# Performance work log

Measured on AMD Instinct MI355X. Metric: run time of the kernel, lower is better.

The kernel has to match this reference:

```python
import jax, jax.numpy as jnp
import numpy as np

HIDDEN = 2048
NUM_HEADS = 32
GROUP_SIZE = 4
HEAD_DIM = HIDDEN // NUM_HEADS            # 64
GROUP_NUM = NUM_HEADS // GROUP_SIZE       # 8 KV heads
B, S = 2, 2048


def setup_inputs() -> dict:
    key = jax.random.key(0)
    ks = jax.random.split(key, 7)
    sc = 1.0 / np.sqrt(HIDDEN)
    x = jax.random.normal(ks[0], (B, S, HIDDEN), dtype=jnp.float32)
    attention_mask = jnp.ones((B, S), dtype=jnp.int32)
    Wq = jax.random.normal(ks[1], (HIDDEN, HIDDEN), dtype=jnp.float32) * sc
    bq = jax.random.normal(ks[2], (HIDDEN,), dtype=jnp.float32) * 0.02
    Wk = jax.random.normal(ks[3], (HIDDEN, GROUP_NUM * HEAD_DIM), dtype=jnp.float32) * sc
    bk = jax.random.normal(ks[4], (GROUP_NUM * HEAD_DIM,), dtype=jnp.float32) * 0.02
    Wv = jax.random.normal(ks[5], (HIDDEN, GROUP_NUM * HEAD_DIM), dtype=jnp.float32) * sc
    bv = jax.random.normal(ks[6], (GROUP_NUM * HEAD_DIM,), dtype=jnp.float32) * 0.02
    return {"x": x, "attention_mask": attention_mask,
            "Wq": Wq, "bq": bq, "Wk": Wk, "bk": bk, "Wv": Wv, "bv": bv}


def reference(x, attention_mask, Wq, bq, Wk, bk, Wv, bv):
    b, s, _ = x.shape
    # projections
    q = (x @ Wq + bq).reshape(b, s, NUM_HEADS, HEAD_DIM).transpose(0, 2, 1, 3)   # (B,H,S,hd)
    k = (x @ Wk + bk).reshape(b, s, GROUP_NUM, HEAD_DIM).transpose(0, 2, 1, 3)   # (B,G,S,hd)
    v = (x @ Wv + bv).reshape(b, s, GROUP_NUM, HEAD_DIM).transpose(0, 2, 1, 3)
    # expand KV groups to full head count (head h uses group h // group_size)
    k = jnp.repeat(k, GROUP_SIZE, axis=1)                                        # (B,H,S,hd)
    v = jnp.repeat(v, GROUP_SIZE, axis=1)
    # NOTE: original torch code uses floor-division `//` for scaling and no softmax
    score = jnp.floor(jnp.einsum('bhqd,bhkd->bhqk', q, k) / np.sqrt(HEAD_DIM).astype(np.float32))
    score = jnp.where(attention_mask[:, None, None, :] == 0, -jnp.inf, score)
    out = jnp.einsum('bhqk,bhkd->bhqd', score, v)                                # (B,H,S,hd)
    return out.transpose(0, 2, 1, 3).reshape(b, s, HIDDEN)
```

## Files before the change

kernel.cpp:

```cpp
#include <hip/hip_runtime.h>
#include <math.h>

#define HIDDEN 2048
#define NHEADS 32
#define HDIM 64
#define GNUM 8
#define KVDIM 512
#define BB 2
#define SS 2048
#define MROWS (BB * SS)
#define NQKV 3072

typedef _Float16 half8 __attribute__((ext_vector_type(8)));
typedef _Float16 half4 __attribute__((ext_vector_type(4)));
typedef _Float16 half2 __attribute__((ext_vector_type(2)));
typedef __fp16 fp16x2 __attribute__((ext_vector_type(2)));
typedef float floatx4 __attribute__((ext_vector_type(4)));

#define MFMA16(a, b, c) __builtin_amdgcn_mfma_f32_16x16x32_f16((a), (b), (c), 0, 0, 0)

__device__ __forceinline__ void split_f32(float x, _Float16& hi, _Float16& lo) {
    hi = (_Float16)x;
    lo = (_Float16)((x - (float)hi) * 2048.0f);
}

__device__ __forceinline__ void load_lds16(const void* g, void* l) {
    __builtin_amdgcn_global_load_lds(
        (const __attribute__((address_space(1))) void*)g,
        (__attribute__((address_space(3))) void*)l, 16, 0, 0);
}

__device__ __forceinline__ void permswap32(unsigned& a, unsigned& b) {
    asm volatile("v_permlane32_swap_b32 %0, %1" : "+v"(a), "+v"(b));
}
__device__ __forceinline__ void permswap16(unsigned& a, unsigned& b) {
    asm volatile("v_permlane16_swap_b32 %0, %1" : "+v"(a), "+v"(b));
}

__device__ __forceinline__ unsigned pk_f16(float a, float b) {
    union { fp16x2 h; unsigned u; } c;
    c.h = __builtin_amdgcn_cvt_pkrtz(a, b);
    return c.u;
}

__global__ __launch_bounds__(256)
void split_x(const float* __restrict__ x, _Float16* __restrict__ xh,
             _Float16* __restrict__ xl, int n4) {
    for (int idx = blockIdx.x * 256 + threadIdx.x; idx < n4; idx += gridDim.x * 256) {
        floatx4 v = reinterpret_cast<const floatx4*>(x)[idx];
        half4 h, l;
        #pragma unroll
        for (int e = 0; e < 4; ++e) { _Float16 hi, lo; split_f32(v[e], hi, lo); h[e] = hi; l[e] = lo; }
        reinterpret_cast<half4*>(xh)[idx] = h;
        reinterpret_cast<half4*>(xl)[idx] = l;
    }
}

__global__ __launch_bounds__(256)
void split_wt(const float* __restrict__ W, int N, int n0,
              _Float16* __restrict__ Wth, _Float16* __restrict__ Wtl) {
    __shared__ float tile[64][68];
    const int tid = threadIdx.x;
    const int kb = blockIdx.x, nb = blockIdx.y;
    #pragma unroll
    for (int i = 0; i < 4; ++i) {
        int idx = tid + i * 256;
        int r = idx >> 4, c4 = idx & 15;
        floatx4 v = *reinterpret_cast<const floatx4*>(&W[(size_t)(kb * 64 + r) * N + nb * 64 + c4 * 4]);
        *reinterpret_cast<floatx4*>(&tile[r][c4 * 4]) = v;
    }
    __syncthreads();
    #pragma unroll
    for (int i = 0; i < 4; ++i) {
        int idx = tid + i * 256;
        int r2 = idx >> 4, c2 = (idx & 15) * 4;
        half4 h, l;
        #pragma unroll
        for (int e = 0; e < 4; ++e) {
            _Float16 hi, lo;
            split_f32(tile[c2 + e][r2], hi, lo);
            h[e] = hi; l[e] = lo;
        }
        size_t o = (size_t)(n0 + nb * 64 + r2) * HIDDEN + kb * 64 + c2;
        *reinterpret_cast<half4*>(&Wth[o]) = h;
        *reinterpret_cast<half4*>(&Wtl[o]) = l;
    }
}

__global__ __launch_bounds__(256)
void biascat_k(const float* __restrict__ bq, const float* __restrict__ bk,
               const float* __restrict__ bv, float* __restrict__ bias) {
    int i = blockIdx.x * 256 + threadIdx.x;
    if (i < 2048) bias[i] = bq[i];
    else if (i < 2560) bias[i] = bk[i - 2048];
    else if (i < NQKV) bias[i] = bv[i - 2560];
}

__global__ __launch_bounds__(256, 2)
void gemm_qkv(const _Float16* __restrict__ xh, const _Float16* __restrict__ xl,
              const _Float16* __restrict__ Wth, const _Float16* __restrict__ Wtl,
              const float* __restrict__ bias,
              _Float16* __restrict__ qh, _Float16* __restrict__ ql,
              _Float16* __restrict__ khs, _Float16* __restrict__ kls,
              _Float16* __restrict__ vhs) {
    __shared__ __align__(16) _Float16 Ah[128 * 64];
    __shared__ __align__(16) _Float16 Al[128 * 64];
    __shared__ __align__(16) _Float16 Bh[128 * 64];
    __shared__ __align__(16) _Float16 Bl[128 * 64];

    const int tid  = threadIdx.x;
    const int lane = tid & 63;
    const int w    = tid >> 6;
    const int wm   = w >> 1, wn = w & 1;
    const int bm   = blockIdx.x, bn = blockIdx.y;
    const int ml   = lane & 15;
    const int kg8  = (lane >> 4) * 8;
    const bool lo3 = (bn < 20);

    const _Float16* gsrc;
    _Float16* ldst;
    if      (w == 0) { gsrc = xh  + (size_t)(bm * 128) * HIDDEN; ldst = Ah; }
    else if (w == 1) { gsrc = xl  + (size_t)(bm * 128) * HIDDEN; ldst = Al; }
    else if (w == 2) { gsrc = Wth + (size_t)(bn * 128) * HIDDEN; ldst = Bh; }
    else             { gsrc = Wtl + (size_t)(bn * 128) * HIDDEN; ldst = Bl; }
    const bool do_stage = lo3 || (w == 0) || (w == 2);

    floatx4 acc0[4][4] = {};
    floatx4 accL[4][4] = {};

    for (int k0 = 0; k0 < HIDDEN; k0 += 64) {
        if (do_stage) {
            #pragma unroll
            for (int i = 0; i < 16; ++i) {
                int L   = i * 1024 + lane * 16;
                int row = L >> 7;
                int off = (L & 127) ^ ((row & 7) << 4);
                const void* gp = (const char*)(gsrc + (size_t)row * HIDDEN + k0) + off;
                void* lp = (char*)ldst + i * 1024;
                load_lds16(gp, lp);
            }
        }
        __syncthreads();

        #pragma unroll
        for (int kc = 0; kc < 2; ++kc) {
            half8 a_h[4], b_h[4];
            #pragma unroll
            for (int r = 0; r < 4; ++r) {
                int row = wm * 64 + r * 16 + ml;
                int byt = row * 128 + (((kc * 64 + kg8 * 2)) ^ ((row & 7) << 4));
                a_h[r] = *reinterpret_cast<const half8*>((const char*)Ah + byt);
            }
            #pragma unroll
            for (int c = 0; c < 4; ++c) {
                int row = wn * 64 + c * 16 + ml;
                int byt = row * 128 + (((kc * 64 + kg8 * 2)) ^ ((row & 7) << 4));
                b_h[c] = *reinterpret_cast<const half8*>((const char*)Bh + byt);
            }
            if (lo3) {
                half8 a_l[4], b_l[4];
                #pragma unroll
                for (int r = 0; r < 4; ++r) {
                    int row = wm * 64 + r * 16 + ml;
                    int byt = row * 128 + (((kc * 64 + kg8 * 2)) ^ ((row & 7) << 4));
                    a_l[r] = *reinterpret_cast<const half8*>((const char*)Al + byt);
                }
                #pragma unroll
                for (int c = 0; c < 4; ++c) {
                    int row = wn * 64 + c * 16 + ml;
                    int byt = row * 128 + (((kc * 64 + kg8 * 2)) ^ ((row & 7) << 4));
                    b_l[c] = *reinterpret_cast<const half8*>((const char*)Bl + byt);
                }
                #pragma unroll
                for (int r = 0; r < 4; ++r)
                    #pragma unroll
                    for (int c = 0; c < 4; ++c) {
                        acc0[r][c] = MFMA16(a_h[r], b_h[c], acc0[r][c]);
                        accL[r][c] = MFMA16(a_h[r], b_l[c], accL[r][c]);
                        accL[r][c] = MFMA16(a_l[r], b_h[c], accL[r][c]);
                    }
            } else {
                #pragma unroll
                for (int r = 0; r < 4; ++r)
                    #pragma unroll
                    for (int c = 0; c < 4; ++c)
                        acc0[r][c] = MFMA16(a_h[r], b_h[c], acc0[r][c]);
            }
        }
        __syncthreads();
    }

    #pragma unroll
    for (int c = 0; c < 4; ++c) {
        int colg = bn * 128 + wn * 64 + c * 16 + ml;
        float bval = bias[colg];
        #pragma unroll
        for (int r = 0; r < 4; ++r) {
            int rowg = bm * 128 + wm * 64 + r * 16 + (lane >> 4) * 4;
            #pragma unroll
            for (int reg = 0; reg < 4; ++reg) {
                float val = acc0[r][c][reg] + accL[r][c][reg] * (1.0f / 2048.0f) + bval;
                int rr = rowg + reg;
                if (colg < 2048) {
                    _Float16 hi, lo; split_f32(val, hi, lo);
                    qh[(size_t)rr * HIDDEN + colg] = hi;
                    ql[(size_t)rr * HIDDEN + colg] = lo;
                } else if (colg < 2560) {
                    int ck = colg - 2048;
                    int gk = ck >> 6, dk = ck & 63;
                    int bk_ = rr >> 11, sk_ = rr & 2047;
                    int kk = sk_ & 63;
                    size_t baseK = ((size_t)((bk_ * 8 + gk) * 32 + (sk_ >> 6))) * 4096
                                 + kk * 64 + (dk ^ ((kk & 7) << 3));
                    _Float16 hi, lo; split_f32(val, hi, lo);
                    khs[baseK] = hi;
                    kls[baseK] = lo;
                } else {
                    int ck = colg - 2560;
                    int gk = ck >> 6, dk = ck & 63;
                    int bk_ = rr >> 11, sk_ = rr & 2047;
                    int s6 = sk_ & 63;
                    size_t baseV = ((size_t)((bk_ * 8 + gk) * 32 + (sk_ >> 6))) * 4096
                                 + dk * 64 + (s6 ^ ((dk & 7) << 3));
                    vhs[baseV] = (_Float16)val;
                }
            }
        }
    }
}

__global__ __launch_bounds__(256, 2)
void attn7(const _Float16* __restrict__ qh, const _Float16* __restrict__ ql,
           const _Float16* __restrict__ khs, const _Float16* __restrict__ kls,
           const _Float16* __restrict__ vhs, const int* __restrict__ mask,
           float* __restrict__ out) {
    __shared__ __align__(16) _Float16 Ksh[64 * 64];
    __shared__ __align__(16) _Float16 Ksl[64 * 64];
    __shared__ __align__(16) _Float16 Vs[64 * 64];

    const int tid  = threadIdx.x;
    const int lane = tid & 63;
    const int w    = tid >> 6;
    const int ml   = lane & 15;
    const int lg   = lane >> 4;
    const int kg8  = lg * 8;

    const int f_  = blockIdx.y * 32 + blockIdx.x;
    const int bg  = (f_ & 7) | ((f_ >> 8) << 3);
    const int qt  = (f_ >> 3) & 31;
    const int b   = bg >> 3, g = bg & 7;

    half8 qhf[4][2], qlf[4][2];
    {
        size_t rowbase = (size_t)(b * SS + qt * 64 + w * 16 + ml) * HIDDEN;
        #pragma unroll
        for (int hh = 0; hh < 4; ++hh) {
            int hcol = (g * 4 + hh) * HDIM;
            #pragma unroll
            for (int gch = 0; gch < 2; ++gch) {
                half8 a = *reinterpret_cast<const half8*>(&qh[rowbase + hcol + gch * 32 + kg8]);
                half8 c = *reinterpret_cast<const half8*>(&ql[rowbase + hcol + gch * 32 + kg8]);
                qhf[hh][gch] = a * (_Float16)0.125f;
                qlf[hh][gch] = c * (_Float16)0.125f;
            }
        }
    }

    const _Float16* ktile_h = khs + (size_t)(bg * 32) * 4096;
    const _Float16* ktile_l = kls + (size_t)(bg * 32) * 4096;
    const _Float16* vtile   = vhs + (size_t)(bg * 32) * 4096;
    const int* mb = mask + b * SS;

    floatx4 oacc[4][4] = {};

    for (int kt = 0; kt < SS / 64; ++kt) {
        __syncthreads();
        if (w == 0) {
            #pragma unroll
            for (int j = 0; j < 8; ++j)
                load_lds16((const char*)(ktile_h + (size_t)kt * 4096) + j * 1024 + lane * 16,
                           (char*)Ksh + j * 1024);
        } else if (w == 1) {
            #pragma unroll
            for (int j = 0; j < 8; ++j)
                load_lds16((const char*)(ktile_l + (size_t)kt * 4096) + j * 1024 + lane * 16,
                           (char*)Ksl + j * 1024);
        } else if (w == 2) {
            #pragma unroll
            for (int j = 0; j < 8; ++j)
                load_lds16((const char*)(vtile + (size_t)kt * 4096) + j * 1024 + lane * 16,
                           (char*)Vs + j * 1024);
        }
        __syncthreads();

        half8 av[4][2];
        #pragma unroll
        for (int f = 0; f < 4; ++f) {
            int vrow = f * 16 + ml;
            int vxo = (vrow & 7) << 3;
            #pragma unroll
            for (int kc = 0; kc < 2; ++kc)
                av[f][kc] = *reinterpret_cast<const half8*>(
                    &Vs[vrow * 64 + ((kc * 32 + kg8) ^ vxo)]);
        }

        int4 m4v[4];
        #pragma unroll
        for (int fc = 0; fc < 4; ++fc)
            m4v[fc] = *reinterpret_cast<const int4*>(&mb[kt * 64 + fc * 16 + lg * 4]);

        __builtin_amdgcn_s_setprio(1);

        unsigned h2[4][4][2];
        #pragma unroll
        for (int fc = 0; fc < 4; ++fc) {
            int krow = fc * 16 + ml;
            int xo = (krow & 7) << 3;
            half8 k_h[2], k_l[2];
            #pragma unroll
            for (int gch = 0; gch < 2; ++gch) {
                k_h[gch] = *reinterpret_cast<const half8*>(&Ksh[krow * 64 + ((gch * 32 + kg8) ^ xo)]);
                k_l[gch] = *reinterpret_cast<const half8*>(&Ksl[krow * 64 + ((gch * 32 + kg8) ^ xo)]);
            }
            #pragma unroll
            for (int hh = 0; hh < 4; ++hh) {
                floatx4 s0 = {}, sl = {};
                s0 = MFMA16(k_h[0], qhf[hh][0], s0);
                s0 = MFMA16(k_h[1], qhf[hh][1], s0);
                sl = MFMA16(k_l[0], qhf[hh][0], sl);
                sl = MFMA16(k_l[1], qhf[hh][1], sl);
                sl = MFMA16(k_h[0], qlf[hh][0], sl);
                sl = MFMA16(k_h[1], qlf[hh][1], sl);
                float sv[4];
                #pragma unroll
                for (int r = 0; r < 4; ++r) {
                    float t = floorf(fmaf(sl[r], 1.0f / 2048.0f, s0[r]));
                    sv[r] = (m4v[fc][r] == 0) ? -INFINITY : t;
                }
                h2[hh][fc][0] = pk_f16(sv[0], sv[1]);
                h2[hh][fc][1] = pk_f16(sv[2], sv[3]);
            }
        }

        #pragma unroll
        for (int hh = 0; hh < 4; ++hh) {
            #pragma unroll
            for (int kc = 0; kc < 2; ++kc) {
                unsigned t0 = h2[hh][2 * kc][0], tA = h2[hh][2 * kc + 1][0];
                unsigned t1 = h2[hh][2 * kc][1], tB = h2[hh][2 * kc + 1][1];
                permswap32(t0, tA); permswap16(t0, tA);
                permswap32(t1, tB); permswap16(t1, tB);
                union { unsigned u[4]; half8 h; } bu;
                bu.u[0] = t0; bu.u[1] = t1; bu.u[2] = tA; bu.u[3] = tB;
                #pragma unroll
                for (int f = 0; f < 4; ++f)
                    oacc[hh][f] = MFMA16(av[f][kc], bu.h, oacc[hh][f]);
            }
        }
        __builtin_amdgcn_s_setprio(0);
    }

    #pragma unroll
    for (int hh = 0; hh < 4; ++hh) {
        int hcol = (g * 4 + hh) * HDIM;
        #pragma unroll
        for (int f = 0; f < 4; ++f) {
            size_t row = (size_t)(b * SS + qt * 64 + w * 16 + ml);
            *reinterpret_cast<floatx4*>(&out[row * HIDDEN + hcol + f * 16 + lg * 4]) = oacc[hh][f];
        }
    }
}

extern "C" void kernel_launch(void* const* d_in, const int* in_sizes, int n_in,
                              void* d_out, int out_size, void* d_ws, size_t ws_size,
                              hipStream_t stream) {
    (void)in_sizes; (void)n_in; (void)out_size; (void)ws_size;
    const float* x    = (const float*)d_in[0];
    const int*   mask = (const int*)d_in[1];
    const float* Wq   = (const float*)d_in[2];
    const float* bq   = (const float*)d_in[3];
    const float* Wk   = (const float*)d_in[4];
    const float* bk   = (const float*)d_in[5];
    const float* Wv   = (const float*)d_in[6];
    const float* bv   = (const float*)d_in[7];

    _Float16* ws16 = (_Float16*)d_ws;
    size_t o = 0;
    auto alloc16 = [&](size_t n) { _Float16* p = ws16 + o; o += n; return p; };
    _Float16* xh  = alloc16((size_t)MROWS * HIDDEN);
    _Float16* xl  = alloc16((size_t)MROWS * HIDDEN);
    _Float16* Wth = alloc16((size_t)NQKV * HIDDEN);
    _Float16* Wtl = alloc16((size_t)NQKV * HIDDEN);
    _Float16* qh  = alloc16((size_t)MROWS * HIDDEN);
    _Float16* ql  = alloc16((size_t)MROWS * HIDDEN);
    _Float16* khs = alloc16((size_t)MROWS * KVDIM);
    _Float16* kls = alloc16((size_t)MROWS * KVDIM);
    _Float16* vhs = alloc16((size_t)MROWS * KVDIM);
    float* biascat = (float*)(ws16 + o);

    split_x<<<2048, 256, 0, stream>>>(x, xh, xl, MROWS * HIDDEN / 4);
    split_wt<<<dim3(32, 32), 256, 0, stream>>>(Wq, HIDDEN, 0,    Wth, Wtl);
    split_wt<<<dim3(32, 8),  256, 0, stream>>>(Wk, KVDIM, 2048, Wth, Wtl);
    split_wt<<<dim3(32, 8),  256, 0, stream>>>(Wv, KVDIM, 2560, Wth, Wtl);
    biascat_k<<<12, 256, 0, stream>>>(bq, bk, bv, biascat);
    gemm_qkv<<<dim3(MROWS / 128, NQKV / 128), 256, 0, stream>>>(
        xh, xl, Wth, Wtl, biascat, qh, ql, khs, kls, vhs);
    attn7<<<dim3(32, 16), 256, 0, stream>>>(qh, ql, khs, kls, vhs, mask, (float*)d_out);
}
```

Baseline: 298.8 us.

## Merge hi/lo QKV GEMM accumulators via prescaled fp16 operands and halve K tile

The QKV projection GEMM now uses a single accumulator array instead of separate hi and lo accumulators. It pre-scales the hi operands by 1/32 so the cross terms can be summed directly into the main accumulator, and the split scale factor drops from 2048 to 32 to match. The K tile is halved to 32, which halves shared memory use, and the loop keeps one barrier before staging. The aim is to free accumulator registers and LDS, at the cost of twice as many K iterations and barriers and reduced precision for the low-part correction.

```diff
diff --git a/kernel.cpp b/kernel.cpp
--- a/kernel.cpp
+++ b/kernel.cpp
@@ -21,7 +21,7 @@
 
 __device__ __forceinline__ void split_f32(float x, _Float16& hi, _Float16& lo) {
     hi = (_Float16)x;
-    lo = (_Float16)((x - (float)hi) * 2048.0f);
+    lo = (_Float16)((x - (float)hi) * 32.0f);
 }
 
 __device__ __forceinline__ void load_lds16(const void* g, void* l) {
@@ -103,10 +103,10 @@
               _Float16* __restrict__ qh, _Float16* __restrict__ ql,
               _Float16* __restrict__ khs, _Float16* __restrict__ kls,
               _Float16* __restrict__ vhs) {
-    __shared__ __align__(16) _Float16 Ah[128 * 64];
-    __shared__ __align__(16) _Float16 Al[128 * 64];
-    __shared__ __align__(16) _Float16 Bh[128 * 64];
-    __shared__ __align__(16) _Float16 Bl[128 * 64];
+    __shared__ __align__(16) _Float16 Ah[128 * 32];
+    __shared__ __align__(16) _Float16 Al[128 * 32];
+    __shared__ __align__(16) _Float16 Bh[128 * 32];
+    __shared__ __align__(16) _Float16 Bl[128 * 32];
 
     const int tid  = threadIdx.x;
     const int lane = tid & 63;
@@ -125,69 +125,66 @@
     else             { gsrc = Wtl + (size_t)(bn * 128) * HIDDEN; ldst = Bl; }
     const bool do_stage = lo3 || (w == 0) || (w == 2);
 
-    floatx4 acc0[4][4] = {};
-    floatx4 accL[4][4] = {};
-
-    for (int k0 = 0; k0 < HIDDEN; k0 += 64) {
+    floatx4 acc[4][4] = {};
+    const _Float16 inv32 = (_Float16)0.03125f;
+
+    for (int t = 0; t < HIDDEN / 32; ++t) {
+        __syncthreads();
         if (do_stage) {
-            #pragma unroll
-            for (int i = 0; i < 16; ++i) {
+            const int k0 = t * 32;
+            #pragma unroll
+            for (int i = 0; i < 8; ++i) {
                 int L   = i * 1024 + lane * 16;
-                int row = L >> 7;
-                int off = (L & 127) ^ ((row & 7) << 4);
-                const void* gp = (const char*)(gsrc + (size_t)row * HIDDEN + k0) + off;
-                void* lp = (char*)ldst + i * 1024;
-                load_lds16(gp, lp);
+                int row = L >> 6;
+                int off = (L & 63) ^ (((row >> 1) & 3) << 4);
+                load_lds16((const char*)(gsrc + (size_t)row * HIDDEN + k0) + off,
+                           ldst + i * 512);
             }
         }
         __syncthreads();
 
-        #pragma unroll
-        for (int kc = 0; kc < 2; ++kc) {
-            half8 a_h[4], b_h[4];
+        if (lo3) {
+            half8 b_h[4], b_l[4], bh32[4];
+            #pragma unroll
+            for (int c = 0; c < 4; ++c) {
+                int row = wn * 64 + c * 16 + ml;
+                int byt = row * 64 + ((kg8 * 2) ^ (((row >> 1) & 3) << 4));
+                b_h[c] = *reinterpret_cast<const half8*>((const char*)Bh + byt);
+                b_l[c] = *reinterpret_cast<const half8*>((const char*)Bl + byt);
+                bh32[c] = b_h[c] * inv32;
+            }
             #pragma unroll
             for (int r = 0; r < 4; ++r) {
                 int row = wm * 64 + r * 16 + ml;
-                int byt = row * 128 + (((kc * 64 + kg8 * 2)) ^ ((row & 7) << 4));
-                a_h[r] = *reinterpret_cast<const half8*>((const char*)Ah + byt);
-            }
+                int byt = row * 64 + ((kg8 * 2) ^ (((row >> 1) & 3) << 4));
+                half8 a_h = *reinterpret_cast<const half8*>((const char*)Ah + byt);
+                half8 a_l = *reinterpret_cast<const half8*>((const char*)Al + byt);
+                half8 ah32 = a_h * inv32;
+                #pragma unroll
+                for (int c = 0; c < 4; ++c) {
+                    acc[r][c] = MFMA16(a_h,  b_h[c],  acc[r][c]);
+                    acc[r][c] = MFMA16(ah32, b_l[c],  acc[r][c]);
+                    acc[r][c] = MFMA16(a_l,  bh32[c], acc[r][c]);
+                }
+            }
+        } else {
+            half8 b_h[4];
             #pragma unroll
             for (int c = 0; c < 4; ++c) {
                 int row = wn * 64 + c * 16 + ml;
-                int byt = row * 128 + (((kc * 64 + kg8 * 2)) ^ ((row & 7) << 4));
+                int byt = row * 64 + ((kg8 * 2) ^ (((row >> 1) & 3) << 4));
                 b_h[c] = *reinterpret_cast<const half8*>((const char*)Bh + byt);
             }
-            if (lo3) {
-                half8 a_l[4], b_l[4];
+            #pragma unroll
+            for (int r = 0; r < 4; ++r) {
+                int row = wm * 64 + r * 16 + ml;
+                int byt = row * 64 + ((kg8 * 2) ^ (((row >> 1) & 3) << 4));
+                half8 a_h = *reinterpret_cast<const half8*>((const char*)Ah + byt);
                 #pragma unroll
-                for (int r = 0; r < 4; ++r) {
-                    int row = wm * 64 + r * 16 + ml;
-                    int byt = row * 128 + (((kc * 64 + kg8 * 2)) ^ ((row & 7) << 4));
-                    a_l[r] = *reinterpret_cast<const half8*>((const char*)Al + byt);
-                }
-                #pragma unroll
-                for (int c = 0; c < 4; ++c) {
-                    int row = wn * 64 + c * 16 + ml;
-                    int byt = row * 128 + (((kc * 64 + kg8 * 2)) ^ ((row & 7) << 4));
-                    b_l[c] = *reinterpret_cast<const half8*>((const char*)Bl + byt);
-                }
-                #pragma unroll
-                for (int r = 0; r < 4; ++r)
-                    #pragma unroll
-                    for (int c = 0; c < 4; ++c) {
-                        acc0[r][c] = MFMA16(a_h[r], b_h[c], acc0[r][c]);
-                        accL[r][c] = MFMA16(a_h[r], b_l[c], accL[r][c]);
-                        accL[r][c] = MFMA16(a_l[r], b_h[c], accL[r][c]);
-                    }
-            } else {
-                #pragma unroll
-                for (int r = 0; r < 4; ++r)
-                    #pragma unroll
-                    for (int c = 0; c < 4; ++c)
-                        acc0[r][c] = MFMA16(a_h[r], b_h[c], acc0[r][c]);
-            }
-        }
-        __syncthreads();
+                for (int c = 0; c < 4; ++c)
+                    acc[r][c] = MFMA16(a_h, b_h[c], acc[r][c]);
+            }
+        }
     }
 
     #pragma unroll
@@ -199,7 +196,7 @@
             int rowg = bm * 128 + wm * 64 + r * 16 + (lane >> 4) * 4;
             #pragma unroll
             for (int reg = 0; reg < 4; ++reg) {
-                float val = acc0[r][c][reg] + accL[r][c][reg] * (1.0f / 2048.0f) + bval;
+                float val = acc[r][c][reg] + bval;
                 int rr = rowg + reg;
                 if (colg < 2048) {
                     _Float16 hi, lo; split_f32(val, hi, lo);
@@ -334,7 +331,7 @@
                 float sv[4];
                 #pragma unroll
                 for (int r = 0; r < 4; ++r) {
-                    float t = floorf(fmaf(sl[r], 1.0f / 2048.0f, s0[r]));
+                    float t = floorf(fmaf(sl[r], 1.0f / 32.0f, s0[r]));
                     sv[r] = (m4v[fc][r] == 0) ? -INFINITY : t;
                 }
                 h2[hh][fc][0] = pk_f16(sv[0], sv[1]);
```

Result: slower. 311.3 us (+4.2%).
